# Performance work log

Measured on AMD Instinct MI355X. Metric: run time of the kernel, lower is better.

Reference implementation:

```python
import jax, jax.numpy as jnp
import numpy as np

N_QUBITS = 8
N_LAYERS = 4
BATCH = 8192


def _ry_mat(theta):
    # RY(theta) = [[cos(t/2), -sin(t/2)], [sin(t/2), cos(t/2)]]; theta scalar or (B,)
    c = jnp.cos(theta * 0.5)
    s = jnp.sin(theta * 0.5)
    return jnp.stack([jnp.stack([c, -s], -1), jnp.stack([s, c], -1)], -2).astype(jnp.complex64)


def _apply_1q(state, U, wire):
    # U: (2,2) gate shared across batch; state: (B, 2,...,2) with axis wire+1 = target wire
    s = jnp.moveaxis(state, wire + 1, -1)
    s = jnp.einsum('ij,...j->...i', U, s)
    return jnp.moveaxis(s, -1, wire + 1)


def _apply_1q_batched(state, U, wire):
    # U: (B,2,2) per-sample gate (data-dependent RY angles)
    s = jnp.moveaxis(state, wire + 1, -1)
    s = jnp.einsum('bij,b...j->b...i', U, s)
    return jnp.moveaxis(s, -1, wire + 1)


def _apply_rz(state, theta, wire):
    # RZ is diagonal: multiply amplitudes by exp(-i t/2) / exp(+i t/2)
    phases = jnp.stack([jnp.exp(-0.5j * theta), jnp.exp(0.5j * theta)]).astype(jnp.complex64)
    s = jnp.moveaxis(state, wire + 1, -1)
    s = s * phases
    return jnp.moveaxis(s, -1, wire + 1)


def _cnot(state, c, t):
    # flip target amplitudes on the control=1 subspace
    s = jnp.moveaxis(state, (c + 1, t + 1), (-2, -1))
    s = jnp.stack([s[..., 0, :], s[..., 1, ::-1]], axis=-2)
    return jnp.moveaxis(s, (-2, -1), (c + 1, t + 1))


def _forward(x, weights):
    B = x.shape[0]
    state = jnp.zeros((B,) + (2,) * N_QUBITS, jnp.complex64)
    state = state.at[(slice(None),) + (0,) * N_QUBITS].set(1.0)  # |0...0>
    # data-encoding RY layer (angles depend on inputs -> per-sample gates)
    for i in range(N_QUBITS):
        state = _apply_1q_batched(state, _ry_mat(x[:, i] + weights[0, i, 0]), i)
    # entangling + rotation layers
    for layer in range(N_LAYERS):
        for i in range(N_QUBITS - 1):
            state = _cnot(state, i, i + 1)
        state = _cnot(state, N_QUBITS - 1, 0)
        for i in range(N_QUBITS):
            state = _apply_rz(state, weights[layer, i, 1], i)
            state = _apply_1q(state, _ry_mat(weights[layer, i, 0]), i)
    # <Z_i> = p(wire_i = 0) - p(wire_i = 1)
    p = state.real ** 2 + state.imag ** 2
    all_axes = tuple(range(1, N_QUBITS + 1))
    outs = []
    for i in range(N_QUBITS):
        m = p.sum(axis=tuple(a for a in all_axes if a != i + 1))  # (B, 2)
        outs.append(m[:, 0] - m[:, 1])
    return jnp.stack(outs, axis=1)  # (B, N_QUBITS)


def setup_inputs() -> dict:
    key = jax.random.key(0)
    k1, k2 = jax.random.split(key)
    x = jax.random.normal(k1, (BATCH, N_QUBITS), jnp.float32)
    weights = jax.random.normal(k2, (N_LAYERS, N_QUBITS, 2), jnp.float32)
    return {"x": x, "weights": weights}


def reference(x, weights):
    return _forward(x, weights)
```

## Files before the change

### kernel.cpp

```cpp
#include <hip/hip_runtime.h>

#define BATCH 8192

typedef __attribute__((ext_vector_type(8))) short bf16x8;
typedef __attribute__((ext_vector_type(4))) float f32x4;

__device__ __forceinline__ unsigned short f2bf(float f) {
    unsigned int u = __float_as_uint(f);
    u += 0x7fffu + ((u >> 16) & 1u);
    return (unsigned short)(u >> 16);
}
__device__ __forceinline__ float rdl(float v, int lane) {
    return __int_as_float(__builtin_amdgcn_readlane(__float_as_int(v), lane));
}

__global__ __launch_bounds__(64) void ukern(const float* __restrict__ w,
                                            unsigned short* __restrict__ Ub)
{
    const int l = threadIdx.x;
    const int c = blockIdx.x;

    float v0, v1, v2, v3;
    {
        const int t  = l & 31;
        const int li = t >> 3;
        const int wi = t & 7;
        float th = w[(li * 8 + wi) * 2 + 0];
        float ph = w[(li * 8 + wi) * 2 + 1];
        float cth = __cosf(0.5f * th), sth = __sinf(0.5f * th);
        if (wi < 6) {
            float cph = __cosf(0.5f * ph), sph = __sinf(0.5f * ph);
            v0 = cth * cph;
            v1 = cth * sph;
            v2 = sth * cph;
            v3 = sth * sph;
        } else {
            v0 = cth;
            v1 = sth;
            v2 = __cosf(ph);
            v3 = __sinf(ph);
        }
    }

    float re[4], im[4];
    const bool ls = (l == (c >> 2));
    #pragma unroll
    for (int k = 0; k < 4; ++k) {
        re[k] = (ls && ((c & 3) == k)) ? 1.0f : 0.0f;
        im[k] = 0.0f;
    }
    const int  src = (l ^ (l >> 1)) & 63;
    const bool c5  = (l & 1);

    #pragma unroll
    for (int layer = 0; layer < 4; ++layer) {
        const int lb = layer * 8;
        float tr[4], ti[4];
        #pragma unroll
        for (int k = 0; k < 4; ++k) {
            tr[k] = __shfl(re[k], src, 64);
            ti[k] = __shfl(im[k], src, 64);
        }
        re[0] = c5 ? tr[2] : tr[0];  im[0] = c5 ? ti[2] : ti[0];
        re[1] = c5 ? tr[3] : tr[1];  im[1] = c5 ? ti[3] : ti[1];
        re[2] = c5 ? tr[1] : tr[3];  im[2] = c5 ? ti[1] : ti[3];
        re[3] = c5 ? tr[0] : tr[2];  im[3] = c5 ? ti[0] : ti[2];
        re[1] = __shfl_xor(re[1], 32, 64); im[1] = __shfl_xor(im[1], 32, 64);
        re[3] = __shfl_xor(re[3], 32, 64); im[3] = __shfl_xor(im[3], 32, 64);

        #pragma unroll
        for (int i = 0; i < 6; ++i) {
            float Ar = rdl(v0, lb + i);
            float SZ = rdl(v3, lb + i);
            float sgn = (l & (32 >> i)) ? 1.0f : -1.0f;
            float Ai = sgn * rdl(v1, lb + i);
            float Br = sgn * rdl(v2, lb + i);
            const int m = 32 >> i;
            #pragma unroll
            for (int k = 0; k < 4; ++k) {
                float br = __shfl_xor(re[k], m, 64);
                float bi = __shfl_xor(im[k], m, 64);
                float ar = re[k], ai = im[k];
                re[k] = Ar*ar - Ai*ai + Br*br + SZ*bi;
                im[k] = Ar*ai + Ai*ar + Br*bi - SZ*br;
            }
        }
        #pragma unroll
        for (int i = 0; i < 2; ++i) {
            float cy = rdl(v0, lb + 6 + i);
            float sy = rdl(v1, lb + 6 + i);
            float cf = rdl(v2, lb + 6 + i);
            float sf = rdl(v3, lb + 6 + i);
            const int mk = 2 >> i;
            #pragma unroll
            for (int k = 0; k < 4; ++k) {
                if (!(k & mk)) continue;
                float r = re[k], q = im[k];
                re[k] = r * cf - q * sf;
                im[k] = q * cf + r * sf;
            }
            #pragma unroll
            for (int k = 0; k < 4; ++k) {
                if (k & mk) continue;
                int k1 = k | mk;
                float ar = re[k], ai = im[k], br = re[k1], bi = im[k1];
                re[k]  = cy * ar - sy * br;
                im[k]  = cy * ai - sy * bi;
                re[k1] = sy * ar + cy * br;
                im[k1] = sy * ai + cy * bi;
            }
        }
    }
    #pragma unroll
    for (int k = 0; k < 4; ++k) {
        int i = l * 4 + k;
        Ub[i * 256 + c]         = f2bf(re[k]);
        Ub[(256 + i) * 256 + c] = f2bf(im[k]);
    }
}

__global__ __launch_bounds__(512) void qmain(const float* __restrict__ x,
                                             const float* __restrict__ w,
                                             const unsigned short* __restrict__ Ub,
                                             float* __restrict__ out)
{
    __shared__ float trg[32][17];
    __shared__ unsigned short psi[32 * 264];
    __shared__ float Ps[8][289];
    const int tid  = threadIdx.x;
    const int wid  = tid >> 6;
    const int lane = tid & 63;
    const int bid  = blockIdx.x;
    const int s0   = bid * 32;

    if (tid < 256) {
        const int s  = tid >> 3;
        const int wi = tid & 7;
        float a = 0.5f * (x[(s0 + s) * 8 + wi] + w[2 * wi]);
        trg[s][wi]     = __cosf(a);
        trg[s][8 + wi] = __sinf(a);
    }
    __syncthreads();

    {
        const int s  = tid >> 4;
        const int j1 = tid & 15;
        float c0 = trg[s][0], c1 = trg[s][1], c2 = trg[s][2], c3 = trg[s][3];
        float s0w = trg[s][8], s1w = trg[s][9], s2w = trg[s][10], s3w = trg[s][11];
        float A1 = ((j1 & 8) ? s0w : c0) * ((j1 & 4) ? s1w : c1)
                 * ((j1 & 2) ? s2w : c2) * ((j1 & 1) ? s3w : c3);
        float c4 = trg[s][4], c5 = trg[s][5], c6 = trg[s][6], c7 = trg[s][7];
        float s4 = trg[s][12], s5 = trg[s][13], s6 = trg[s][14], s7 = trg[s][15];
        float q45[4] = {A1 * c4 * c5, A1 * c4 * s5, A1 * s4 * c5, A1 * s4 * s5};
        float p67[4] = {c6 * c7, c6 * s7, s6 * c7, s6 * s7};
        unsigned int wbuf[8];
        #pragma unroll
        for (int p = 0; p < 8; ++p) {
            int ja = 2 * p, jb = 2 * p + 1;
            float va = q45[ja >> 2] * p67[ja & 3];
            float vb = q45[jb >> 2] * p67[jb & 3];
            wbuf[p] = (unsigned int)f2bf(va) | ((unsigned int)f2bf(vb) << 16);
        }
        uint4* dst = (uint4*)((char*)psi + s * 528 + j1 * 32);
        dst[0] = make_uint4(wbuf[0], wbuf[1], wbuf[2], wbuf[3]);
        dst[1] = make_uint4(wbuf[4], wbuf[5], wbuf[6], wbuf[7]);
    }
    __syncthreads();

    const int mrow = lane & 15;
    const int kgrp = lane >> 4;

    f32x4 acc[4][2];
    #pragma unroll
    for (int a = 0; a < 4; ++a)
        #pragma unroll
        for (int b = 0; b < 2; ++b)
            acc[a][b] = (f32x4){0.f, 0.f, 0.f, 0.f};

    #pragma unroll
    for (int ks = 0; ks < 8; ++ks) {
        const int k0 = ks * 32 + kgrp * 8;
        bf16x8 bfr0 = *(const bf16x8*)(psi + mrow * 264 + k0);
        bf16x8 bfr1 = *(const bf16x8*)(psi + (16 + mrow) * 264 + k0);
        #pragma unroll
        for (int mt = 0; mt < 4; ++mt) {
            const int row = (mt < 2) ? (wid * 32 + mt * 16 + mrow)
                                     : (256 + wid * 32 + (mt - 2) * 16 + mrow);
            bf16x8 afr = *(const bf16x8*)(Ub + row * 256 + k0);
            acc[mt][0] = __builtin_amdgcn_mfma_f32_16x16x32_bf16(afr, bfr0, acc[mt][0], 0, 0, 0);
            acc[mt][1] = __builtin_amdgcn_mfma_f32_16x16x32_bf16(afr, bfr1, acc[mt][1], 0, 0, 0);
        }
    }

    #pragma unroll
    for (int nt = 0; nt < 2; ++nt) {
        float am[2], r2m[2], r1m[2];
        #pragma unroll
        for (int mtl = 0; mtl < 2; ++mtl) {
            float p0 = acc[mtl][nt][0]*acc[mtl][nt][0] + acc[mtl+2][nt][0]*acc[mtl+2][nt][0];
            float p1 = acc[mtl][nt][1]*acc[mtl][nt][1] + acc[mtl+2][nt][1]*acc[mtl+2][nt][1];
            float p2 = acc[mtl][nt][2]*acc[mtl][nt][2] + acc[mtl+2][nt][2]*acc[mtl+2][nt][2];
            float p3 = acc[mtl][nt][3]*acc[mtl][nt][3] + acc[mtl+2][nt][3]*acc[mtl+2][nt][3];
            float t0 = p0 + p1, t1 = p2 + p3;
            am[mtl]  = t0 + t1;
            r2m[mtl] = t0 - t1;
            r1m[mtl] = (p0 - p1) + (p2 - p3);
        }
        float ps = am[0] + am[1];
        float m3 = am[0] - am[1];
        float m6 = r2m[0] + r2m[1];
        float m7 = r1m[0] + r1m[1];
        float m0 = (wid & 4)  ? -ps : ps;
        float m1 = (wid & 2)  ? -ps : ps;
        float m2 = (wid & 1)  ? -ps : ps;
        float m4 = (kgrp & 2) ? -ps : ps;
        float m5 = (kgrp & 1) ? -ps : ps;
        m0 += __shfl_xor(m0, 16, 64);  m0 += __shfl_xor(m0, 32, 64);
        m1 += __shfl_xor(m1, 16, 64);  m1 += __shfl_xor(m1, 32, 64);
        m2 += __shfl_xor(m2, 16, 64);  m2 += __shfl_xor(m2, 32, 64);
        m3 += __shfl_xor(m3, 16, 64);  m3 += __shfl_xor(m3, 32, 64);
        m4 += __shfl_xor(m4, 16, 64);  m4 += __shfl_xor(m4, 32, 64);
        m5 += __shfl_xor(m5, 16, 64);  m5 += __shfl_xor(m5, 32, 64);
        m6 += __shfl_xor(m6, 16, 64);  m6 += __shfl_xor(m6, 32, 64);
        m7 += __shfl_xor(m7, 16, 64);  m7 += __shfl_xor(m7, 32, 64);
        if (kgrp == 0) {
            const int snt = nt * 16 + mrow;
            float* pp = &Ps[wid][snt * 9];
            pp[0]=m0; pp[1]=m1; pp[2]=m2; pp[3]=m3; pp[4]=m4; pp[5]=m5; pp[6]=m6; pp[7]=m7;
        }
    }
    __syncthreads();
    if (tid < 64) {
        const int s    = tid & 31;
        const int half = tid >> 5;
        float r0 = 0.f, r1 = 0.f, r2 = 0.f, r3 = 0.f;
        #pragma unroll
        for (int uu = 0; uu < 8; ++uu) {
            const float* pp = &Ps[uu][s * 9 + half * 4];
            r0 += pp[0]; r1 += pp[1]; r2 += pp[2]; r3 += pp[3];
        }
        float4* o = (float4*)(out + (s0 + s) * 8 + half * 4);
        *o = make_float4(r0, r1, r2, r3);
    }
}

extern "C" void kernel_launch(void* const* d_in, const int* in_sizes, int n_in,
                              void* d_out, int out_size, void* d_ws, size_t ws_size,
                              hipStream_t stream)
{
    const float* x = (const float*)d_in[0];
    const float* w = (const float*)d_in[1];
    unsigned short* Ub = (unsigned short*)d_ws;
    ukern<<<256, 64, 0, stream>>>(w, Ub);
    qmain<<<256, 512, 0, stream>>>(x, w, Ub, (float*)d_out);
}
```

Baseline: 22.15 us.

## Split unitary rows across two blocks per sample tile and combine with atomics

The main kernel now launches twice as many blocks. Each block covers half of the 256 output amplitude rows for its 32 samples, which halves the MFMA work and accumulators per warp. Partial expectation values are combined into the output with float atomicAdd, so a memset of the output is added before the launches. This raises parallelism across the 256 CUs, but each block repeats the input encoding, and the change adds a memset launch and atomic traffic.

```diff
diff --git a/kernel.cpp b/kernel.cpp
--- a/kernel.cpp
+++ b/kernel.cpp
@@ -30,15 +30,9 @@
         float cth = __cosf(0.5f * th), sth = __sinf(0.5f * th);
         if (wi < 6) {
             float cph = __cosf(0.5f * ph), sph = __sinf(0.5f * ph);
-            v0 = cth * cph;
-            v1 = cth * sph;
-            v2 = sth * cph;
-            v3 = sth * sph;
+            v0 = cth * cph;  v1 = cth * sph;  v2 = sth * cph;  v3 = sth * sph;
         } else {
-            v0 = cth;
-            v1 = sth;
-            v2 = __cosf(ph);
-            v3 = __sinf(ph);
+            v0 = cth;  v1 = sth;  v2 = __cosf(ph);  v3 = __sinf(ph);
         }
     }
 
@@ -130,8 +124,9 @@
     const int tid  = threadIdx.x;
     const int wid  = tid >> 6;
     const int lane = tid & 63;
-    const int bid  = blockIdx.x;
-    const int s0   = bid * 32;
+    const int sb   = blockIdx.x & 255;
+    const int half = blockIdx.x >> 8;
+    const int s0   = sb * 32;
 
     if (tid < 256) {
         const int s  = tid >> 3;
@@ -169,10 +164,11 @@
 
     const int mrow = lane & 15;
     const int kgrp = lane >> 4;
-
-    f32x4 acc[4][2];
-    #pragma unroll
-    for (int a = 0; a < 4; ++a)
+    const int aw0  = half * 128 + wid * 16;
+
+    f32x4 acc[2][2];
+    #pragma unroll
+    for (int a = 0; a < 2; ++a)
         #pragma unroll
         for (int b = 0; b < 2; ++b)
             acc[a][b] = (f32x4){0.f, 0.f, 0.f, 0.f};
@@ -182,37 +178,28 @@
         const int k0 = ks * 32 + kgrp * 8;
         bf16x8 bfr0 = *(const bf16x8*)(psi + mrow * 264 + k0);
         bf16x8 bfr1 = *(const bf16x8*)(psi + (16 + mrow) * 264 + k0);
-        #pragma unroll
-        for (int mt = 0; mt < 4; ++mt) {
-            const int row = (mt < 2) ? (wid * 32 + mt * 16 + mrow)
-                                     : (256 + wid * 32 + (mt - 2) * 16 + mrow);
-            bf16x8 afr = *(const bf16x8*)(Ub + row * 256 + k0);
-            acc[mt][0] = __builtin_amdgcn_mfma_f32_16x16x32_bf16(afr, bfr0, acc[mt][0], 0, 0, 0);
-            acc[mt][1] = __builtin_amdgcn_mfma_f32_16x16x32_bf16(afr, bfr1, acc[mt][1], 0, 0, 0);
-        }
+        bf16x8 afr0 = *(const bf16x8*)(Ub + (aw0 + mrow) * 256 + k0);
+        bf16x8 afr1 = *(const bf16x8*)(Ub + (256 + aw0 + mrow) * 256 + k0);
+        acc[0][0] = __builtin_amdgcn_mfma_f32_16x16x32_bf16(afr0, bfr0, acc[0][0], 0, 0, 0);
+        acc[0][1] = __builtin_amdgcn_mfma_f32_16x16x32_bf16(afr0, bfr1, acc[0][1], 0, 0, 0);
+        acc[1][0] = __builtin_amdgcn_mfma_f32_16x16x32_bf16(afr1, bfr0, acc[1][0], 0, 0, 0);
+        acc[1][1] = __builtin_amdgcn_mfma_f32_16x16x32_bf16(afr1, bfr1, acc[1][1], 0, 0, 0);
     }
 
     #pragma unroll
     for (int nt = 0; nt < 2; ++nt) {
-        float am[2], r2m[2], r1m[2];
-        #pragma unroll
-        for (int mtl = 0; mtl < 2; ++mtl) {
-            float p0 = acc[mtl][nt][0]*acc[mtl][nt][0] + acc[mtl+2][nt][0]*acc[mtl+2][nt][0];
-            float p1 = acc[mtl][nt][1]*acc[mtl][nt][1] + acc[mtl+2][nt][1]*acc[mtl+2][nt][1];
-            float p2 = acc[mtl][nt][2]*acc[mtl][nt][2] + acc[mtl+2][nt][2]*acc[mtl+2][nt][2];
-            float p3 = acc[mtl][nt][3]*acc[mtl][nt][3] + acc[mtl+2][nt][3]*acc[mtl+2][nt][3];
-            float t0 = p0 + p1, t1 = p2 + p3;
-            am[mtl]  = t0 + t1;
-            r2m[mtl] = t0 - t1;
-            r1m[mtl] = (p0 - p1) + (p2 - p3);
-        }
-        float ps = am[0] + am[1];
-        float m3 = am[0] - am[1];
-        float m6 = r2m[0] + r2m[1];
-        float m7 = r1m[0] + r1m[1];
-        float m0 = (wid & 4)  ? -ps : ps;
-        float m1 = (wid & 2)  ? -ps : ps;
-        float m2 = (wid & 1)  ? -ps : ps;
+        float p0 = acc[0][nt][0]*acc[0][nt][0] + acc[1][nt][0]*acc[1][nt][0];
+        float p1 = acc[0][nt][1]*acc[0][nt][1] + acc[1][nt][1]*acc[1][nt][1];
+        float p2 = acc[0][nt][2]*acc[0][nt][2] + acc[1][nt][2]*acc[1][nt][2];
+        float p3 = acc[0][nt][3]*acc[0][nt][3] + acc[1][nt][3]*acc[1][nt][3];
+        float t0 = p0 + p1, t1 = p2 + p3;
+        float ps = t0 + t1;
+        float m6 = t0 - t1;
+        float m7 = (p0 - p1) + (p2 - p3);
+        float m0 = half       ? -ps : ps;
+        float m1 = (wid & 4)  ? -ps : ps;
+        float m2 = (wid & 2)  ? -ps : ps;
+        float m3 = (wid & 1)  ? -ps : ps;
         float m4 = (kgrp & 2) ? -ps : ps;
         float m5 = (kgrp & 1) ? -ps : ps;
         m0 += __shfl_xor(m0, 16, 64);  m0 += __shfl_xor(m0, 32, 64);
@@ -231,16 +218,19 @@
     }
     __syncthreads();
     if (tid < 64) {
-        const int s    = tid & 31;
-        const int half = tid >> 5;
+        const int s  = tid & 31;
+        const int hq = tid >> 5;
         float r0 = 0.f, r1 = 0.f, r2 = 0.f, r3 = 0.f;
         #pragma unroll
         for (int uu = 0; uu < 8; ++uu) {
-            const float* pp = &Ps[uu][s * 9 + half * 4];
+            const float* pp = &Ps[uu][s * 9 + hq * 4];
             r0 += pp[0]; r1 += pp[1]; r2 += pp[2]; r3 += pp[3];
         }
-        float4* o = (float4*)(out + (s0 + s) * 8 + half * 4);
-        *o = make_float4(r0, r1, r2, r3);
+        float* o = out + (s0 + s) * 8 + hq * 4;
+        atomicAdd(o + 0, r0);
+        atomicAdd(o + 1, r1);
+        atomicAdd(o + 2, r2);
+        atomicAdd(o + 3, r3);
     }
 }
 
@@ -251,6 +241,7 @@
     const float* x = (const float*)d_in[0];
     const float* w = (const float*)d_in[1];
     unsigned short* Ub = (unsigned short*)d_ws;
+    hipMemsetAsync(d_out, 0, (size_t)out_size * sizeof(float), stream);
     ukern<<<256, 64, 0, stream>>>(w, Ub);
-    qmain<<<256, 512, 0, stream>>>(x, w, Ub, (float*)d_out);
-}
+    qmain<<<512, 512, 0, stream>>>(x, w, Ub, (float*)d_out);
+}
```

New measurement: 27.21 us. +22.9%, slower.

## Store U matrix in MFMA fragment-tiled layout and prefetch A fragments

Applied to the files above, without the earlier changes.

The unitary-building kernel now writes the bf16 U matrix into a tiled layout where each 16x32 MFMA A-fragment sits in one contiguous 1 KB block. Each lane's 16-byte load is then contiguous across the wavefront instead of strided by rows of 256 elements. The main kernel also loads the next k-step's four A fragments before issuing the current MFMAs, a software pipeline that hides global load latency. The cost is more live registers and more involved index arithmetic.

```diff
diff --git a/kernel.cpp b/kernel.cpp
--- a/kernel.cpp
+++ b/kernel.cpp
@@ -30,15 +30,9 @@
         float cth = __cosf(0.5f * th), sth = __sinf(0.5f * th);
         if (wi < 6) {
             float cph = __cosf(0.5f * ph), sph = __sinf(0.5f * ph);
-            v0 = cth * cph;
-            v1 = cth * sph;
-            v2 = sth * cph;
-            v3 = sth * sph;
+            v0 = cth * cph;  v1 = cth * sph;  v2 = sth * cph;  v3 = sth * sph;
         } else {
-            v0 = cth;
-            v1 = sth;
-            v2 = __cosf(ph);
-            v3 = __sinf(ph);
+            v0 = cth;  v1 = sth;  v2 = __cosf(ph);  v3 = __sinf(ph);
         }
     }
 
@@ -111,11 +105,13 @@
             }
         }
     }
+    const int cterm = (c >> 5) * 512 + ((c >> 3) & 3) * 128 + (c & 7);
     #pragma unroll
     for (int k = 0; k < 4; ++k) {
         int i = l * 4 + k;
-        Ub[i * 256 + c]         = f2bf(re[k]);
-        Ub[(256 + i) * 256 + c] = f2bf(im[k]);
+        int base = (i >> 4) * 4096 + (i & 15) * 8 + cterm;
+        Ub[base]         = f2bf(re[k]);
+        Ub[base + 65536] = f2bf(im[k]);
     }
 }
 
@@ -169,6 +165,8 @@
 
     const int mrow = lane & 15;
     const int kgrp = lane >> 4;
+    const int t0   = wid * 2;
+    const unsigned short* A = Ub + kgrp * 128 + mrow * 8;
 
     f32x4 acc[4][2];
     #pragma unroll
@@ -177,19 +175,33 @@
         for (int b = 0; b < 2; ++b)
             acc[a][b] = (f32x4){0.f, 0.f, 0.f, 0.f};
 
+    bf16x8 a0 = *(const bf16x8*)(A + (t0     ) * 4096);
+    bf16x8 a1 = *(const bf16x8*)(A + (t0 +  1) * 4096);
+    bf16x8 a2 = *(const bf16x8*)(A + (t0 + 16) * 4096);
+    bf16x8 a3 = *(const bf16x8*)(A + (t0 + 17) * 4096);
+
     #pragma unroll
     for (int ks = 0; ks < 8; ++ks) {
+        bf16x8 n0 = a0, n1 = a1, n2 = a2, n3 = a3;
+        if (ks < 7) {
+            const int nk = (ks + 1) * 512;
+            n0 = *(const bf16x8*)(A + (t0     ) * 4096 + nk);
+            n1 = *(const bf16x8*)(A + (t0 +  1) * 4096 + nk);
+            n2 = *(const bf16x8*)(A + (t0 + 16) * 4096 + nk);
+            n3 = *(const bf16x8*)(A + (t0 + 17) * 4096 + nk);
+        }
         const int k0 = ks * 32 + kgrp * 8;
         bf16x8 bfr0 = *(const bf16x8*)(psi + mrow * 264 + k0);
         bf16x8 bfr1 = *(const bf16x8*)(psi + (16 + mrow) * 264 + k0);
-        #pragma unroll
-        for (int mt = 0; mt < 4; ++mt) {
-            const int row = (mt < 2) ? (wid * 32 + mt * 16 + mrow)
-                                     : (256 + wid * 32 + (mt - 2) * 16 + mrow);
-            bf16x8 afr = *(const bf16x8*)(Ub + row * 256 + k0);
-            acc[mt][0] = __builtin_amdgcn_mfma_f32_16x16x32_bf16(afr, bfr0, acc[mt][0], 0, 0, 0);
-            acc[mt][1] = __builtin_amdgcn_mfma_f32_16x16x32_bf16(afr, bfr1, acc[mt][1], 0, 0, 0);
-        }
+        acc[0][0] = __builtin_amdgcn_mfma_f32_16x16x32_bf16(a0, bfr0, acc[0][0], 0, 0, 0);
+        acc[0][1] = __builtin_amdgcn_mfma_f32_16x16x32_bf16(a0, bfr1, acc[0][1], 0, 0, 0);
+        acc[1][0] = __builtin_amdgcn_mfma_f32_16x16x32_bf16(a1, bfr0, acc[1][0], 0, 0, 0);
+        acc[1][1] = __builtin_amdgcn_mfma_f32_16x16x32_bf16(a1, bfr1, acc[1][1], 0, 0, 0);
+        acc[2][0] = __builtin_amdgcn_mfma_f32_16x16x32_bf16(a2, bfr0, acc[2][0], 0, 0, 0);
+        acc[2][1] = __builtin_amdgcn_mfma_f32_16x16x32_bf16(a2, bfr1, acc[2][1], 0, 0, 0);
+        acc[3][0] = __builtin_amdgcn_mfma_f32_16x16x32_bf16(a3, bfr0, acc[3][0], 0, 0, 0);
+        acc[3][1] = __builtin_amdgcn_mfma_f32_16x16x32_bf16(a3, bfr1, acc[3][1], 0, 0, 0);
+        a0 = n0; a1 = n1; a2 = n2; a3 = n3;
     }
 
     #pragma unroll
@@ -201,9 +213,9 @@
             float p1 = acc[mtl][nt][1]*acc[mtl][nt][1] + acc[mtl+2][nt][1]*acc[mtl+2][nt][1];
             float p2 = acc[mtl][nt][2]*acc[mtl][nt][2] + acc[mtl+2][nt][2]*acc[mtl+2][nt][2];
             float p3 = acc[mtl][nt][3]*acc[mtl][nt][3] + acc[mtl+2][nt][3]*acc[mtl+2][nt][3];
-            float t0 = p0 + p1, t1 = p2 + p3;
-            am[mtl]  = t0 + t1;
-            r2m[mtl] = t0 - t1;
+            float t0s = p0 + p1, t1s = p2 + p3;
+            am[mtl]  = t0s + t1s;
+            r2m[mtl] = t0s - t1s;
             r1m[mtl] = (p0 - p1) + (p2 - p3);
         }
         float ps = am[0] + am[1];
```

Result: faster. 19.32 us, median of 2 (-12.7%).
